# Performance work log

Hardware: AMD Instinct MI355X
Metric: run time of the kernel (lower is better)

The kernel has to match this reference:

```python
import jax, jax.numpy as jnp
import numpy as np

BIG = 1000000.0


def setup_inputs() -> dict:
    key = jax.random.key(0)
    k1, k2 = jax.random.split(key)
    embeddings = jax.random.normal(k1, (8192, 128), dtype=jnp.float32)
    labels = jax.random.randint(k2, (8192,), 0, 512, dtype=jnp.int64)
    return {"embeddings": embeddings, "labels": labels, "margin": jnp.float32(0.5)}


def _pairwise_euclidean(x):
    # [N, N] Euclidean distance matrix, numerically safe sqrt (zero diag)
    sq = jnp.sum(x * x, axis=1)
    d2 = sq[:, None] + sq[None, :] - 2.0 * (x @ x.T)
    d2 = jnp.maximum(d2, 0.0)
    nz = d2 > 0.0
    return jnp.where(nz, jnp.sqrt(jnp.where(nz, d2, 1.0)), 0.0)


def reference(embeddings, labels, margin):
    n = embeddings.shape[0]
    dist = _pairwise_euclidean(embeddings)                      # [N, N]
    same = (labels[:, None] == labels[None, :]).astype(dist.dtype)
    mask_pos = same - jnp.eye(n, dtype=dist.dtype)              # positives, excl. self
    mask_neg = 1.0 - same                                       # different label
    pos_dist = jnp.max(dist * mask_pos, axis=1)                 # hardest positive
    neg_dist = jnp.min(dist + (1.0 - mask_neg) * BIG, axis=1)   # hardest negative
    loss = jax.nn.relu(pos_dist - neg_dist + margin)
    return jnp.mean(loss)
```

## Files before the change

### kernel.cpp

```cpp
#include <hip/hip_runtime.h>
#include <hip/hip_bf16.h>

#define NROW 8192
#define DIM  128
#define BI   128
#define BJ   128
#define JSPLIT 8
#define LSTR 136
#define BIGF 1e30f

typedef __attribute__((ext_vector_type(8))) short bf16x8;
typedef __attribute__((ext_vector_type(4))) float f32x4;


__device__ __forceinline__ unsigned short f2bf(float f) {
    unsigned u = __float_as_uint(f);
    unsigned r = (u + 0x7fffu + ((u >> 16) & 1u)) >> 16;
    return (unsigned short)r;
}

__global__ __launch_bounds__(256) void prep_kernel(const float* __restrict__ x,
                                                   unsigned short* __restrict__ xb,
                                                   float* __restrict__ sq,
                                                   unsigned* __restrict__ posb,
                                                   unsigned* __restrict__ negb,
                                                   float* __restrict__ out) {
    int gtid = blockIdx.x * 256 + threadIdx.x;
    if (gtid < NROW) {
        posb[gtid] = 0u;
        negb[gtid] = __float_as_uint(BIGF);
    }
    if (gtid == 0) out[0] = 0.0f;
    int row  = gtid >> 6;
    int lane = threadIdx.x & 63;
    const float* xr = x + (size_t)row * DIM;
    float a = xr[lane];
    float b = xr[lane + 64];
    xb[(size_t)row * DIM + lane]      = f2bf(a);
    xb[(size_t)row * DIM + lane + 64] = f2bf(b);
    float s = a * a + b * b;
    #pragma unroll
    for (int o = 32; o > 0; o >>= 1) s += __shfl_down(s, o);
    if (lane == 0) sq[row] = s;
}

__global__ __launch_bounds__(256, 2) void tri_mfma(const unsigned short* __restrict__ xb,
                                                   const int* __restrict__ lbl,
                                                   const float* __restrict__ sq,
                                                   unsigned* __restrict__ posb,
                                                   unsigned* __restrict__ negb) {
    __shared__ unsigned short As[BI * LSTR];
    __shared__ unsigned short Bs[BJ * LSTR];

    const int bid = blockIdx.x;
    const int rb  = bid >> 3;
    const int jq  = bid & 7;
    const int i0  = rb * BI;
    const int t    = threadIdx.x;
    const int lane = t & 63;
    const int w    = t >> 6;
    const int wrow = (w >> 1) * 64;
    const int wcol = (w & 1) * 64;
    const int quad = lane >> 4;
    const int l15  = lane & 15;

    {
        const int srow = t >> 4;
        const int schk = t & 15;
        #pragma unroll
        for (int it = 0; it < 8; it++) {
            int row = srow + it * 16;
            uint4 v = *(const uint4*)(xb + (size_t)(i0 + row) * DIM + schk * 8);
            *(uint4*)(&As[row * LSTR + schk * 8]) = v;
        }
    }

    float sqi[4][4];
    int   lbli[4][4];
    #pragma unroll
    for (int ti = 0; ti < 4; ti++) {
        int rbase = i0 + wrow + ti * 16 + quad * 4;
        float4 s4 = *(const float4*)(sq + rbase);
        int4   l4 = *(const int4*)(lbl + rbase);
        sqi[ti][0] = s4.x; sqi[ti][1] = s4.y; sqi[ti][2] = s4.z; sqi[ti][3] = s4.w;
        lbli[ti][0] = l4.x; lbli[ti][1] = l4.y; lbli[ti][2] = l4.z; lbli[ti][3] = l4.w;
    }

    float posm[4][4], negm[4][4];
    #pragma unroll
    for (int ti = 0; ti < 4; ti++)
        #pragma unroll
        for (int r = 0; r < 4; r++) { posm[ti][r] = -BIGF; negm[ti][r] = BIGF; }

    #pragma unroll 1
    for (int jt = 0; jt < (NROW / JSPLIT) / BJ; jt++) {
        const int j0 = jq * (NROW / JSPLIT) + jt * BJ;
        __syncthreads();
        {
            const int srow = t >> 4;
            const int schk = t & 15;
            #pragma unroll
            for (int it = 0; it < 8; it++) {
                int row = srow + it * 16;
                uint4 v = *(const uint4*)(xb + (size_t)(j0 + row) * DIM + schk * 8);
                *(uint4*)(&Bs[row * LSTR + schk * 8]) = v;
            }
        }
        __syncthreads();

        float sqj[4]; int lblj[4];
        #pragma unroll
        for (int tj = 0; tj < 4; tj++) {
            int c = j0 + wcol + tj * 16 + l15;
            sqj[tj]  = sq[c];
            lblj[tj] = lbl[c];
        }

        f32x4 acc[4][4];
        #pragma unroll
        for (int ti = 0; ti < 4; ti++)
            #pragma unroll
            for (int tj = 0; tj < 4; tj++) acc[ti][tj] = (f32x4){0.f, 0.f, 0.f, 0.f};

        #pragma unroll
        for (int ks = 0; ks < 4; ks++) {
            bf16x8 af[4], bfr[4];
            #pragma unroll
            for (int ti = 0; ti < 4; ti++)
                af[ti] = *(const bf16x8*)(&As[(wrow + ti * 16 + l15) * LSTR + ks * 32 + quad * 8]);
            #pragma unroll
            for (int tj = 0; tj < 4; tj++)
                bfr[tj] = *(const bf16x8*)(&Bs[(wcol + tj * 16 + l15) * LSTR + ks * 32 + quad * 8]);
            #pragma unroll
            for (int ti = 0; ti < 4; ti++)
                #pragma unroll
                for (int tj = 0; tj < 4; tj++)
                    acc[ti][tj] = __builtin_amdgcn_mfma_f32_16x16x32_bf16(af[ti], bfr[tj], acc[ti][tj], 0, 0, 0);
        }

        const bool diag = (i0 + wrow) == (j0 + wcol);
        #pragma unroll
        for (int ti = 0; ti < 4; ti++)
            #pragma unroll
            for (int tj = 0; tj < 4; tj++)
                #pragma unroll
                for (int r = 0; r < 4; r++) {
                    float s = fmaf(-2.0f, acc[ti][tj][r], sqj[tj]);
                    bool same = (lbli[ti][r] == lblj[tj]);
                    bool isd  = diag && (ti == tj) && (quad * 4 + r == l15);
                    float sp = (same && !isd) ? s : -BIGF;
                    float sn = same ? BIGF : s;
                    posm[ti][r] = fmaxf(posm[ti][r], sp);
                    negm[ti][r] = fminf(negm[ti][r], sn);
                }
    }

    #pragma unroll
    for (int ti = 0; ti < 4; ti++)
        #pragma unroll
        for (int r = 0; r < 4; r++) {
            float p = posm[ti][r];
            float n = negm[ti][r];
            #pragma unroll
            for (int m = 8; m >= 1; m >>= 1) {
                p = fmaxf(p, __shfl_xor(p, m));
                n = fminf(n, __shfl_xor(n, m));
            }
            if (l15 == 0) {
                int row = i0 + wrow + ti * 16 + quad * 4 + r;
                float d2p = fmaxf(0.0f, sqi[ti][r] + p);
                float d2n = fmaxf(0.0f, sqi[ti][r] + n);
                atomicMax(&posb[row], __float_as_uint(d2p));
                atomicMin(&negb[row], __float_as_uint(d2n));
            }
        }
}

__global__ __launch_bounds__(256) void tri_final(const unsigned* __restrict__ posb,
                                                 const unsigned* __restrict__ negb,
                                                 const float* __restrict__ margin,
                                                 float* __restrict__ out) {
    int r = blockIdx.x * 256 + threadIdx.x;
    float m = margin[0];
    float p  = sqrtf(__uint_as_float(posb[r]));
    float ng = sqrtf(__uint_as_float(negb[r]));
    float loss = fmaxf(p - ng + m, 0.0f) * (1.0f / (float)NROW);
    #pragma unroll
    for (int o = 32; o > 0; o >>= 1) loss += __shfl_down(loss, o);
    __shared__ float wsum[4];
    int lane = threadIdx.x & 63, wv = threadIdx.x >> 6;
    if (lane == 0) wsum[wv] = loss;
    __syncthreads();
    if (threadIdx.x == 0) atomicAdd(out, wsum[0] + wsum[1] + wsum[2] + wsum[3]);
}

extern "C" void kernel_launch(void* const* d_in, const int* in_sizes, int n_in,
                              void* d_out, int out_size, void* d_ws, size_t ws_size,
                              hipStream_t stream) {
    const float* x      = (const float*)d_in[0];
    const int*   lbl    = (const int*)d_in[1];
    const float* margin = (const float*)d_in[2];
    float* out = (float*)d_out;

    unsigned short* xb = (unsigned short*)d_ws;
    float*    sq   = (float*)((char*)d_ws + (size_t)NROW * DIM * 2);
    unsigned* posb = (unsigned*)((char*)sq + NROW * 4);
    unsigned* negb = posb + NROW;

    prep_kernel<<<2048, 256, 0, stream>>>(x, xb, sq, posb, negb, out);
    tri_mfma<<<64 * JSPLIT, 256, 0, stream>>>(xb, lbl, sq, posb, negb);
    tri_final<<<NROW / 256, 256, 0, stream>>>(posb, negb, margin, out);
}
```

Measured before the change: 92.10 us.

## Sort rows by label, use MFMA-fragment layout and drop LDS staging

Rows are counting-sorted by label so each row's positives form a contiguous band, which lets most 16-column tiles take a cheap negative-only epilogue. Embeddings are written in an MFMA-fragment-major bf16 layout so A fragments stay in registers and B fragments load straight from global memory, removing LDS staging and barriers. Per-row atomics are replaced by per-segment partial stores that the final kernel reduces. The cost is a single-block sort kernel with atomic scatter, plus heavier global/L2 traffic for B fragments.

```diff
diff --git a/kernel.cpp b/kernel.cpp
--- a/kernel.cpp
+++ b/kernel.cpp
@@ -1,12 +1,10 @@
 #include <hip/hip_runtime.h>
-#include <hip/hip_bf16.h>
 
 #define NROW 8192
 #define DIM  128
-#define BI   128
-#define BJ   128
+#define NLBL 512
 #define JSPLIT 8
-#define LSTR 136
+#define NSEG  (JSPLIT * 2)
 #define BIGF 1e30f
 
 typedef __attribute__((ext_vector_type(8))) short bf16x8;
@@ -19,43 +17,78 @@
     return (unsigned short)r;
 }
 
-__global__ __launch_bounds__(256) void prep_kernel(const float* __restrict__ x,
-                                                   unsigned short* __restrict__ xb,
-                                                   float* __restrict__ sq,
-                                                   unsigned* __restrict__ posb,
-                                                   unsigned* __restrict__ negb,
-                                                   float* __restrict__ out) {
-    int gtid = blockIdx.x * 256 + threadIdx.x;
-    if (gtid < NROW) {
-        posb[gtid] = 0u;
-        negb[gtid] = __float_as_uint(BIGF);
-    }
-    if (gtid == 0) out[0] = 0.0f;
-    int row  = gtid >> 6;
-    int lane = threadIdx.x & 63;
-    const float* xr = x + (size_t)row * DIM;
-    float a = xr[lane];
-    float b = xr[lane + 64];
-    xb[(size_t)row * DIM + lane]      = f2bf(a);
-    xb[(size_t)row * DIM + lane + 64] = f2bf(b);
-    float s = a * a + b * b;
-    #pragma unroll
-    for (int o = 32; o > 0; o >>= 1) s += __shfl_down(s, o);
-    if (lane == 0) sq[row] = s;
-}
-
-__global__ __launch_bounds__(256, 2) void tri_mfma(const unsigned short* __restrict__ xb,
-                                                   const int* __restrict__ lbl,
-                                                   const float* __restrict__ sq,
-                                                   unsigned* __restrict__ posb,
-                                                   unsigned* __restrict__ negb) {
-    __shared__ unsigned short As[BI * LSTR];
-    __shared__ unsigned short Bs[BJ * LSTR];
-
+__global__ __launch_bounds__(1024) void prep_sort(const int* __restrict__ lbl,
+                                                  int* __restrict__ binStart,
+                                                  unsigned* __restrict__ cursor,
+                                                  float* __restrict__ out) {
+    __shared__ int hist[NLBL];
+    __shared__ int scan[NLBL];
+    const int t = threadIdx.x;
+    if (t < NLBL) hist[t] = 0;
+    __syncthreads();
+    #pragma unroll
+    for (int k = 0; k < NROW / 1024; k++)
+        atomicAdd(&hist[lbl[t + k * 1024]], 1);
+    __syncthreads();
+    if (t < NLBL) scan[t] = hist[t];
+    __syncthreads();
+    for (int off = 1; off < NLBL; off <<= 1) {
+        int v = 0;
+        if (t < NLBL && t >= off) v = scan[t - off];
+        __syncthreads();
+        if (t < NLBL) scan[t] += v;
+        __syncthreads();
+    }
+    if (t < NLBL) {
+        int st = scan[t] - hist[t];
+        binStart[t] = st;
+        cursor[t]   = (unsigned)st;
+    }
+    if (t == 0) { binStart[NLBL] = NROW; out[0] = 0.0f; }
+}
+
+__global__ __launch_bounds__(256) void prep_scatter(const float* __restrict__ x,
+                                                    const int* __restrict__ lbl,
+                                                    const int* __restrict__ binStart,
+                                                    unsigned* __restrict__ cursor,
+                                                    unsigned short* __restrict__ xb2,
+                                                    float* __restrict__ sq,
+                                                    unsigned* __restrict__ rowBand) {
+    const int t   = threadIdx.x;
+    const int row = blockIdx.x * 16 + (t >> 4);
+    const int c   = t & 15;
+    const float* xr = x + (size_t)row * DIM + c * 8;
+    float4 f0 = *(const float4*)xr;
+    float4 f1 = *(const float4*)(xr + 4);
+    float s = f0.x*f0.x + f0.y*f0.y + f0.z*f0.z + f0.w*f0.w
+            + f1.x*f1.x + f1.y*f1.y + f1.z*f1.z + f1.w*f1.w;
+    #pragma unroll
+    for (int m = 1; m <= 8; m <<= 1) s += __shfl_xor(s, m);
+    const int l = lbl[row];
+    unsigned p = 0;
+    if (c == 0) p = atomicAdd(&cursor[l], 1u);
+    p = __shfl((int)p, t & 48);
+    unsigned w0 = (unsigned)f2bf(f0.x) | ((unsigned)f2bf(f0.y) << 16);
+    unsigned w1 = (unsigned)f2bf(f0.z) | ((unsigned)f2bf(f0.w) << 16);
+    unsigned w2 = (unsigned)f2bf(f1.x) | ((unsigned)f2bf(f1.y) << 16);
+    unsigned w3 = (unsigned)f2bf(f1.z) | ((unsigned)f2bf(f1.w) << 16);
+    uint4 v = make_uint4(w0, w1, w2, w3);
+    *(uint4*)(xb2 + (size_t)(p >> 4) * 2048 + c * 128 + (p & 15) * 8) = v;
+    if (c == 0) {
+        sq[p] = s;
+        rowBand[p] = (unsigned)binStart[l] | ((unsigned)binStart[l + 1] << 16);
+    }
+}
+
+__global__ __launch_bounds__(256, 2) void tile_mfma(const unsigned short* __restrict__ xb2,
+                                                    const float* __restrict__ sq,
+                                                    const unsigned* __restrict__ rowBand,
+                                                    float* __restrict__ posS,
+                                                    float* __restrict__ negS) {
     const int bid = blockIdx.x;
     const int rb  = bid >> 3;
     const int jq  = bid & 7;
-    const int i0  = rb * BI;
+    const int i0  = rb * 128;
     const int t    = threadIdx.x;
     const int lane = t & 63;
     const int w    = t >> 6;
@@ -64,26 +97,37 @@
     const int quad = lane >> 4;
     const int l15  = lane & 15;
 
-    {
-        const int srow = t >> 4;
-        const int schk = t & 15;
-        #pragma unroll
-        for (int it = 0; it < 8; it++) {
-            int row = srow + it * 16;
-            uint4 v = *(const uint4*)(xb + (size_t)(i0 + row) * DIM + schk * 8);
-            *(uint4*)(&As[row * LSTR + schk * 8]) = v;
-        }
-    }
-
-    float sqi[4][4];
-    int   lbli[4][4];
+    bf16x8 af[4][4];
+    const int gA = (i0 + wrow) >> 4;
+    #pragma unroll
+    for (int ti = 0; ti < 4; ti++)
+        #pragma unroll
+        for (int ks = 0; ks < 4; ks++)
+            af[ti][ks] = *(const bf16x8*)(xb2 + (size_t)(gA + ti) * 2048 + (ks * 4 + quad) * 128 + l15 * 8);
+
+    unsigned band[4][4];
     #pragma unroll
     for (int ti = 0; ti < 4; ti++) {
-        int rbase = i0 + wrow + ti * 16 + quad * 4;
-        float4 s4 = *(const float4*)(sq + rbase);
-        int4   l4 = *(const int4*)(lbl + rbase);
-        sqi[ti][0] = s4.x; sqi[ti][1] = s4.y; sqi[ti][2] = s4.z; sqi[ti][3] = s4.w;
-        lbli[ti][0] = l4.x; lbli[ti][1] = l4.y; lbli[ti][2] = l4.z; lbli[ti][3] = l4.w;
+        uint4 b4 = *(const uint4*)(rowBand + i0 + wrow + ti * 16 + quad * 4);
+        band[ti][0] = b4.x; band[ti][1] = b4.y; band[ti][2] = b4.z; band[ti][3] = b4.w;
+    }
+    int tiLo[4], tiHi[4];
+    #pragma unroll
+    for (int ti = 0; ti < 4; ti++) {
+        int lo = (int)(band[ti][0] & 0xffffu), hi = (int)(band[ti][0] >> 16);
+        #pragma unroll
+        for (int r = 1; r < 4; r++) {
+            int l2 = (int)(band[ti][r] & 0xffffu), h2 = (int)(band[ti][r] >> 16);
+            lo = lo < l2 ? lo : l2;
+            hi = hi > h2 ? hi : h2;
+        }
+        int v;
+        v = __shfl_xor(lo, 16); lo = lo < v ? lo : v;
+        v = __shfl_xor(lo, 32); lo = lo < v ? lo : v;
+        v = __shfl_xor(hi, 16); hi = hi > v ? hi : v;
+        v = __shfl_xor(hi, 32); hi = hi > v ? hi : v;
+        tiLo[ti] = __builtin_amdgcn_readfirstlane(lo);
+        tiHi[ti] = __builtin_amdgcn_readfirstlane(hi);
     }
 
     float posm[4][4], negm[4][4];
@@ -92,29 +136,13 @@
         #pragma unroll
         for (int r = 0; r < 4; r++) { posm[ti][r] = -BIGF; negm[ti][r] = BIGF; }
 
+    const int jbase = jq * 1024;
     #pragma unroll 1
-    for (int jt = 0; jt < (NROW / JSPLIT) / BJ; jt++) {
-        const int j0 = jq * (NROW / JSPLIT) + jt * BJ;
-        __syncthreads();
-        {
-            const int srow = t >> 4;
-            const int schk = t & 15;
-            #pragma unroll
-            for (int it = 0; it < 8; it++) {
-                int row = srow + it * 16;
-                uint4 v = *(const uint4*)(xb + (size_t)(j0 + row) * DIM + schk * 8);
-                *(uint4*)(&Bs[row * LSTR + schk * 8]) = v;
-            }
-        }
-        __syncthreads();
-
-        float sqj[4]; int lblj[4];
-        #pragma unroll
-        for (int tj = 0; tj < 4; tj++) {
-            int c = j0 + wcol + tj * 16 + l15;
-            sqj[tj]  = sq[c];
-            lblj[tj] = lbl[c];
-        }
+    for (int jt = 0; jt < 8; jt++) {
+        const int j0 = jbase + jt * 128;
+        float sqj[4];
+        #pragma unroll
+        for (int tj = 0; tj < 4; tj++) sqj[tj] = sq[j0 + wcol + tj * 16 + l15];
 
         f32x4 acc[4][4];
         #pragma unroll
@@ -122,39 +150,50 @@
             #pragma unroll
             for (int tj = 0; tj < 4; tj++) acc[ti][tj] = (f32x4){0.f, 0.f, 0.f, 0.f};
 
+        const int gB = (j0 + wcol) >> 4;
         #pragma unroll
         for (int ks = 0; ks < 4; ks++) {
-            bf16x8 af[4], bfr[4];
-            #pragma unroll
-            for (int ti = 0; ti < 4; ti++)
-                af[ti] = *(const bf16x8*)(&As[(wrow + ti * 16 + l15) * LSTR + ks * 32 + quad * 8]);
+            bf16x8 bfr[4];
             #pragma unroll
             for (int tj = 0; tj < 4; tj++)
-                bfr[tj] = *(const bf16x8*)(&Bs[(wcol + tj * 16 + l15) * LSTR + ks * 32 + quad * 8]);
+                bfr[tj] = *(const bf16x8*)(xb2 + (size_t)(gB + tj) * 2048 + (ks * 4 + quad) * 128 + l15 * 8);
             #pragma unroll
             for (int ti = 0; ti < 4; ti++)
                 #pragma unroll
                 for (int tj = 0; tj < 4; tj++)
-                    acc[ti][tj] = __builtin_amdgcn_mfma_f32_16x16x32_bf16(af[ti], bfr[tj], acc[ti][tj], 0, 0, 0);
-        }
-
-        const bool diag = (i0 + wrow) == (j0 + wcol);
-        #pragma unroll
-        for (int ti = 0; ti < 4; ti++)
-            #pragma unroll
-            for (int tj = 0; tj < 4; tj++)
-                #pragma unroll
-                for (int r = 0; r < 4; r++) {
-                    float s = fmaf(-2.0f, acc[ti][tj][r], sqj[tj]);
-                    bool same = (lbli[ti][r] == lblj[tj]);
-                    bool isd  = diag && (ti == tj) && (quad * 4 + r == l15);
-                    float sp = (same && !isd) ? s : -BIGF;
-                    float sn = same ? BIGF : s;
-                    posm[ti][r] = fmaxf(posm[ti][r], sp);
-                    negm[ti][r] = fminf(negm[ti][r], sn);
+                    acc[ti][tj] = __builtin_amdgcn_mfma_f32_16x16x32_bf16(af[ti][ks], bfr[tj], acc[ti][tj], 0, 0, 0);
+        }
+
+        #pragma unroll
+        for (int ti = 0; ti < 4; ti++) {
+            #pragma unroll
+            for (int tj = 0; tj < 4; tj++) {
+                const int colLo = j0 + wcol + tj * 16;
+                if (colLo + 16 <= tiLo[ti] || colLo >= tiHi[ti]) {
+                    #pragma unroll
+                    for (int r = 0; r < 4; r++) {
+                        float sr = fmaf(-2.0f, acc[ti][tj][r], sqj[tj]);
+                        negm[ti][r] = fminf(negm[ti][r], sr);
+                    }
+                } else {
+                    const int jcol  = colLo + l15;
+                    const int rowg0 = i0 + wrow + ti * 16 + quad * 4;
+                    #pragma unroll
+                    for (int r = 0; r < 4; r++) {
+                        float sr = fmaf(-2.0f, acc[ti][tj][r], sqj[tj]);
+                        const int lo = (int)(band[ti][r] & 0xffffu);
+                        const int hi = (int)(band[ti][r] >> 16);
+                        bool inb  = (jcol >= lo) && (jcol < hi);
+                        bool self = (jcol == rowg0 + r);
+                        posm[ti][r] = fmaxf(posm[ti][r], (inb && !self) ? sr : -BIGF);
+                        negm[ti][r] = fminf(negm[ti][r], inb ? BIGF : sr);
+                    }
                 }
-    }
-
+            }
+        }
+    }
+
+    const int seg = jq * 2 + (wcol >> 6);
     #pragma unroll
     for (int ti = 0; ti < 4; ti++)
         #pragma unroll
@@ -168,23 +207,26 @@
             }
             if (l15 == 0) {
                 int row = i0 + wrow + ti * 16 + quad * 4 + r;
-                float d2p = fmaxf(0.0f, sqi[ti][r] + p);
-                float d2n = fmaxf(0.0f, sqi[ti][r] + n);
-                atomicMax(&posb[row], __float_as_uint(d2p));
-                atomicMin(&negb[row], __float_as_uint(d2n));
+                float sqi = sq[row];
+                posS[seg * NROW + row] = fmaxf(0.0f, sqi + p);
+                negS[seg * NROW + row] = fmaxf(0.0f, sqi + n);
             }
         }
 }
 
-__global__ __launch_bounds__(256) void tri_final(const unsigned* __restrict__ posb,
-                                                 const unsigned* __restrict__ negb,
+__global__ __launch_bounds__(256) void tri_final(const float* __restrict__ posS,
+                                                 const float* __restrict__ negS,
                                                  const float* __restrict__ margin,
                                                  float* __restrict__ out) {
     int r = blockIdx.x * 256 + threadIdx.x;
+    float p = 0.0f, n = BIGF;
+    #pragma unroll
+    for (int q = 0; q < NSEG; q++) {
+        p = fmaxf(p, posS[q * NROW + r]);
+        n = fminf(n, negS[q * NROW + r]);
+    }
     float m = margin[0];
-    float p  = sqrtf(__uint_as_float(posb[r]));
-    float ng = sqrtf(__uint_as_float(negb[r]));
-    float loss = fmaxf(p - ng + m, 0.0f) * (1.0f / (float)NROW);
+    float loss = fmaxf(sqrtf(p) - sqrtf(n) + m, 0.0f) * (1.0f / (float)NROW);
     #pragma unroll
     for (int o = 32; o > 0; o >>= 1) loss += __shfl_down(loss, o);
     __shared__ float wsum[4];
@@ -202,12 +244,17 @@
     const float* margin = (const float*)d_in[2];
     float* out = (float*)d_out;
 
-    unsigned short* xb = (unsigned short*)d_ws;
-    float*    sq   = (float*)((char*)d_ws + (size_t)NROW * DIM * 2);
-    unsigned* posb = (unsigned*)((char*)sq + NROW * 4);
-    unsigned* negb = posb + NROW;
-
-    prep_kernel<<<2048, 256, 0, stream>>>(x, xb, sq, posb, negb, out);
-    tri_mfma<<<64 * JSPLIT, 256, 0, stream>>>(xb, lbl, sq, posb, negb);
-    tri_final<<<NROW / 256, 256, 0, stream>>>(posb, negb, margin, out);
-}
+    char* ws = (char*)d_ws;
+    unsigned short* xb2 = (unsigned short*)ws;
+    float*    sq       = (float*)(ws + (2u << 20));
+    unsigned* rowBand  = (unsigned*)(ws + (2u << 20) + (32u << 10));
+    int*      binStart = (int*)(ws + (2u << 20) + (64u << 10));
+    unsigned* cursor   = (unsigned*)(ws + (2u << 20) + (68u << 10));
+    float*    posS     = (float*)(ws + (2u << 20) + (128u << 10));
+    float*    negS     = (float*)(ws + (2u << 20) + (640u << 10));
+
+    prep_sort<<<1, 1024, 0, stream>>>(lbl, binStart, cursor, out);
+    prep_scatter<<<NROW / 16, 256, 0, stream>>>(x, lbl, binStart, cursor, xb2, sq, rowBand);
+    tile_mfma<<<64 * JSPLIT, 256, 0, stream>>>(xb2, sq, rowBand, posS, negS);
+    tri_final<<<NROW / 256, 256, 0, stream>>>(posS, negS, margin, out);
+}
```

New measurement: 97.58 us. 1.06x slower.
